# Kernel optimization log

Measured on AMD Instinct MI355X. Metric: run time of the kernel, lower is better.

## Reference

```python
import jax, jax.numpy as jnp
import numpy as np
from jax import lax

PRE_NMS_TOP_N = 2000
POST_NMS_TOP_N = 1000
NMS_THRESH = 0.7
MIN_SIZE = 0.0
BBOX_XFORM_CLIP = float(np.log(1000.0 / 16.0))
NEG = jnp.float32(-1e30)


def setup_inputs() -> dict:
    key = jax.random.key(0)
    k1, k2, k3, k4, k5 = jax.random.split(key, 5)
    N, A, H, W = 16, 3, 256, 336
    img_h, img_w = 1024, 1344
    num = A * H * W  # 258048 anchors per image
    objectness = jax.random.normal(k1, (N, A, H, W), jnp.float32)
    box_regression = jax.random.normal(k2, (N, A * 4, H, W), jnp.float32) * 0.5
    # synthetic but valid xyxy anchors (x2 > x1, y2 > y1)
    cx = jax.random.uniform(k3, (N, num)) * img_w
    cy = jax.random.uniform(k4, (N, num)) * img_h
    wh = 16.0 + jax.random.uniform(k5, (N, num, 2)) * 256.0
    anchors = jnp.stack([cx - 0.5 * wh[..., 0], cy - 0.5 * wh[..., 1],
                         cx + 0.5 * wh[..., 0], cy + 0.5 * wh[..., 1]], axis=-1)
    return {"anchors": anchors.astype(jnp.float32), "objectness": objectness,
            "box_regression": box_regression, "img_h": img_h, "img_w": img_w}


def box_decode(codes, anchors):
    # BoxCoder(weights=(1,1,1,1)).decode, TO_REMOVE=1 convention
    w = anchors[..., 2] - anchors[..., 0] + 1.0
    h = anchors[..., 3] - anchors[..., 1] + 1.0
    ctr_x = anchors[..., 0] + 0.5 * w
    ctr_y = anchors[..., 1] + 0.5 * h
    dx, dy, dw, dh = codes[..., 0], codes[..., 1], codes[..., 2], codes[..., 3]
    dw = jnp.minimum(dw, BBOX_XFORM_CLIP)
    dh = jnp.minimum(dh, BBOX_XFORM_CLIP)
    pcx = dx * w + ctr_x
    pcy = dy * h + ctr_y
    pw = jnp.exp(dw) * w
    ph = jnp.exp(dh) * h
    return jnp.stack([pcx - 0.5 * pw, pcy - 0.5 * ph,
                      pcx + 0.5 * pw - 1.0, pcy + 0.5 * ph - 1.0], axis=-1)


def pairwise_iou(boxes):
    area = (boxes[:, 2] - boxes[:, 0] + 1.0) * (boxes[:, 3] - boxes[:, 1] + 1.0)
    lt = jnp.maximum(boxes[:, None, :2], boxes[None, :, :2])  # [K,K,2]
    rb = jnp.minimum(boxes[:, None, 2:], boxes[None, :, 2:])
    wh = jnp.maximum(rb - lt + 1.0, 0.0)
    inter = wh[..., 0] * wh[..., 1]
    return inter / (area[:, None] + area[None, :] - inter)


def nms_keep(boxes, valid):
    # boxes already sorted by score desc; greedy suppression scan over rows
    K = boxes.shape[0]
    iou = pairwise_iou(boxes)  # [K,K]
    idx = jnp.arange(K)

    def body(keep, xs):
        row, i = xs
        sup = keep[i] & (idx > i) & (row > NMS_THRESH)
        return keep & ~sup, None

    keep, _ = lax.scan(body, valid, (iou, idx))
    return keep


def reference(anchors, objectness, box_regression, img_h, img_w):
    N, A, H, W = objectness.shape
    # permute_and_flatten: (N,A,H,W) -> (N, H*W*A)
    obj = jax.nn.sigmoid(jnp.transpose(objectness, (0, 2, 3, 1)).reshape(N, -1))
    breg = jnp.transpose(box_regression.reshape(N, A, 4, H, W), (0, 3, 4, 1, 2)).reshape(N, -1, 4)
    k = min(PRE_NMS_TOP_N, obj.shape[1])
    scores, topk_idx = lax.top_k(obj, k)  # sorted desc
    batch = jnp.arange(N)[:, None]
    breg = breg[batch, topk_idx]        # [N,k,4]
    anc = anchors[batch, topk_idx]      # [N,k,4]
    boxes = box_decode(breg, anc)       # [N,k,4]
    # clip_to_image (TO_REMOVE=1)
    x1 = jnp.clip(boxes[..., 0], 0.0, img_w - 1)
    y1 = jnp.clip(boxes[..., 1], 0.0, img_h - 1)
    x2 = jnp.clip(boxes[..., 2], 0.0, img_w - 1)
    y2 = jnp.clip(boxes[..., 3], 0.0, img_h - 1)
    boxes = jnp.stack([x1, y1, x2, y2], axis=-1)
    # remove_small_boxes as a validity mask (fixed shape)
    ws = x2 - x1 + 1.0
    hs = y2 - y1 + 1.0
    valid = (ws >= MIN_SIZE) & (hs >= MIN_SIZE)
    keep = jax.vmap(nms_keep)(boxes, valid)  # [N,k]
    masked = jnp.where(keep, scores, NEG)
    final_scores, sel = lax.top_k(masked, POST_NMS_TOP_N)  # preserves score order
    final_boxes = boxes[batch, sel]
    # [N, post_nms_top_n, 5]: xyxy + objectness (padded slots have score ~ -1e30)
    return jnp.concatenate([final_boxes, final_scores[..., None]], axis=-1)
```

## Files before the change

kernel.cpp:

```cpp
#include <hip/hip_runtime.h>
#include <stdint.h>

#define NIMG 16
#define AANCH 3
#define HH 256
#define WW 336
#define HWP (HH*WW)
#define NUM (AANCH*HWP)
#define TOTAL (NIMG*NUM)
#define PRE_K 2000
#define POST_K 1000
#define NMS_TH 0.7f
#define NEGV -1e30f
#define CAND_CAP 4096
#define ROWS 2048
#define RWORDS 64
#define CHUNK 4096
#define CBLOCKS (NUM / CHUNK)
#define HPARTS 16
#define HBINS 4096
#define HCHUNK (NUM / HPARTS)

#define WS_HIST 0u
#define WS_COLT 0u
#define WS_CBOX 262144u
#define WS_CSCO 1310720u
#define WS_CUT  4194304u
#define WS_CNT  4194560u
#define WS_CAND 4194816u
#define WS_BOX  4719104u
#define WS_SCO  5243392u
#define WS_RMI  5374464u
#define WS_SEL  5378560u
#define WS_MASK 5444096u

__device__ __forceinline__ uint32_t fkey(float f){
    uint32_t b = __float_as_uint(f);
    return (b & 0x80000000u) ? ~b : (b | 0x80000000u);
}
__device__ __forceinline__ float keyf(uint32_t k){
    uint32_t b = (k & 0x80000000u) ? (k & 0x7FFFFFFFu) : ~k;
    return __uint_as_float(b);
}

__global__ __launch_bounds__(1024) void k_hist(const float* __restrict__ obj,
                                               uint32_t* __restrict__ part,
                                               uint32_t* __restrict__ cnt,
                                               uint32_t* __restrict__ rminit){
    int img = blockIdx.x >> 4;
    int blk = blockIdx.x & 15;
    int tid = threadIdx.x;
    if (blockIdx.x == 0){
        for (int i = tid; i < 32 + NIMG * RWORDS; i += 1024){
            if (i < 32) cnt[i] = 0u;
            else        rminit[i - 32] = 0u;
        }
    }
    __shared__ uint32_t h[HBINS];
    #pragma unroll
    for (int i = 0; i < HBINS / 1024; ++i) h[tid + i * 1024] = 0u;
    __syncthreads();
    const float* base = obj + (size_t)img * NUM + (size_t)blk * HCHUNK;
    for (int e = tid * 4; e < HCHUNK; e += 4096){
        float4 v = *(const float4*)(base + e);
        atomicAdd(&h[fkey(v.x) >> 20], 1u);
        atomicAdd(&h[fkey(v.y) >> 20], 1u);
        atomicAdd(&h[fkey(v.z) >> 20], 1u);
        atomicAdd(&h[fkey(v.w) >> 20], 1u);
    }
    __syncthreads();
    uint32_t* p = part + ((size_t)blockIdx.x) * HBINS;
    #pragma unroll
    for (int i = 0; i < HBINS / 1024; ++i) p[tid + i * 1024] = h[tid + i * 1024];
}

__global__ __launch_bounds__(1024) void k_binsel(const uint32_t* __restrict__ part,
                                                 uint32_t* __restrict__ cut,
                                                 uint32_t* __restrict__ nAout){
    int img = blockIdx.x, tid = threadIdx.x;
    const uint32_t* pb = part + (size_t)img * HPARTS * HBINS;
    int bin0 = HBINS - 4 * (tid + 1);
    uint32_t c0 = 0, c1 = 0, c2 = 0, c3 = 0;
    for (int k = 0; k < HPARTS; ++k){
        const uint4 v = *(const uint4*)(pb + (size_t)k * HBINS + bin0);
        c0 += v.x; c1 += v.y; c2 += v.z; c3 += v.w;
    }
    uint32_t s = c0 + c1 + c2 + c3;
    __shared__ uint32_t ss[1024];
    uint32_t x = s;
    ss[tid] = x; __syncthreads();
    for (int d = 1; d < 1024; d <<= 1){
        uint32_t y = (tid >= d) ? ss[tid - d] : 0u;
        __syncthreads();
        x += y; ss[tid] = x;
        __syncthreads();
    }
    uint32_t incl = x, excl = x - s;
    if (excl < PRE_K && incl >= PRE_K){
        uint32_t c = excl;
        uint32_t cc[4] = {c0, c1, c2, c3};
        for (int j = 3; j >= 0; --j){
            uint32_t cb = c;
            c += cc[j];
            if (c >= PRE_K){
                cut[img] = ((uint32_t)(bin0 + j)) << 20;
                nAout[img] = cb;
                break;
            }
        }
    }
}

__device__ __forceinline__ void emit_candidate(
        uint32_t key, uint32_t f, uint32_t pos, int img,
        const float* __restrict__ anchors, const float* __restrict__ breg,
        float imw, float imh,
        unsigned long long* __restrict__ cand,
        float4* __restrict__ cboxes, float* __restrict__ cscores){
    const float CLIPV = 4.135166556742356f;
    cand[img * CAND_CAP + pos] = ((unsigned long long)key << 32)
        | ((unsigned long long)((~f) & 0x3FFFFu) << 14) | (unsigned long long)pos;
    float logit = keyf(key);
    float sc = 1.0f / (1.0f + expf(-logit));
    const float* an = anchors + ((size_t)img * NUM + f) * 4;
    float ax1 = an[0], ay1 = an[1], ax2 = an[2], ay2 = an[3];
    int a = (int)(f % AANCH); int hw = (int)(f / AANCH);
    size_t bbase = ((size_t)img * 12 + a * 4) * HWP + (size_t)hw;
    float dx = breg[bbase], dy = breg[bbase + HWP];
    float dw = breg[bbase + 2 * (size_t)HWP], dh = breg[bbase + 3 * (size_t)HWP];
    float aw = ax2 - ax1 + 1.0f, ah = ay2 - ay1 + 1.0f;
    float cx = ax1 + 0.5f * aw, cy = ay1 + 0.5f * ah;
    dw = fminf(dw, CLIPV); dh = fminf(dh, CLIPV);
    float pcx = dx * aw + cx, pcy = dy * ah + cy;
    float pw = expf(dw) * aw, ph = expf(dh) * ah;
    float x1 = pcx - 0.5f * pw, y1 = pcy - 0.5f * ph;
    float x2 = pcx + 0.5f * pw - 1.0f, y2 = pcy + 0.5f * ph - 1.0f;
    x1 = fminf(fmaxf(x1, 0.0f), imw - 1.0f);
    y1 = fminf(fmaxf(y1, 0.0f), imh - 1.0f);
    x2 = fminf(fmaxf(x2, 0.0f), imw - 1.0f);
    y2 = fminf(fmaxf(y2, 0.0f), imh - 1.0f);
    bool valid = ((x2 - x1 + 1.0f) >= 0.0f) && ((y2 - y1 + 1.0f) >= 0.0f);
    cboxes[img * CAND_CAP + pos] = make_float4(x1, y1, x2, y2);
    cscores[img * CAND_CAP + pos] = valid ? sc : -sc;
}

__global__ __launch_bounds__(256) void k_compact(const float* __restrict__ obj,
                                                 const uint32_t* __restrict__ cut,
                                                 const uint32_t* __restrict__ nAarr,
                                                 uint32_t* __restrict__ cnt,
                                                 unsigned long long* __restrict__ cand,
                                                 const float* __restrict__ anchors,
                                                 const float* __restrict__ breg,
                                                 const int* __restrict__ pimh,
                                                 const int* __restrict__ pimw,
                                                 float4* __restrict__ cboxes,
                                                 float* __restrict__ cscores){
    int img   = blockIdx.x / CBLOCKS;
    int chunk = blockIdx.x - img * CBLOCKS;
    int base  = img * NUM + chunk * CHUNK;
    __shared__ uint32_t lcA, lcB, gbA, gbB;
    __shared__ uint2 lbuf[CHUNK];
    if (threadIdx.x == 0){ lcA = 0u; lcB = 0u; }
    __syncthreads();
    uint32_t cutv = cut[img];
    uint32_t cutbin = cutv >> 20;
    float4 v[4];
    #pragma unroll
    for (int it = 0; it < 4; ++it)
        v[it] = *(const float4*)(obj + base + it * 1024 + (int)threadIdx.x * 4);
    #pragma unroll
    for (int it = 0; it < 4; ++it){
        int e = it * 1024 + (int)threadIdx.x * 4;
        float vv[4] = {v[it].x, v[it].y, v[it].z, v[it].w};
        #pragma unroll
        for (int q = 0; q < 4; ++q){
            uint32_t k = fkey(vv[q]);
            if (k >= cutv){
                int r = chunk * CHUNK + e + q;
                int a = r / HWP, hw = r - a * HWP;
                uint32_t f = (uint32_t)(hw * AANCH + a);
                if ((k >> 20) > cutbin){
                    uint32_t p = atomicAdd(&lcA, 1u);
                    lbuf[p] = make_uint2(k, f);
                } else {
                    uint32_t p = atomicAdd(&lcB, 1u);
                    lbuf[CHUNK - 1 - p] = make_uint2(k, f);
                }
            }
        }
    }
    __syncthreads();
    if (threadIdx.x == 0){
        gbA = (lcA > 0u) ? atomicAdd(&cnt[img], lcA) : 0u;
        gbB = (lcB > 0u) ? atomicAdd(&cnt[16 + img], lcB) : 0u;
    }
    __syncthreads();
    uint32_t nA  = nAarr[img];
    uint32_t nAp = (nA + 1u) & ~1u;
    float imw = (float)(*pimw), imh = (float)(*pimh);
    uint32_t na = lcA, ga = gbA, nb = lcB, gb = gbB;
    for (uint32_t t = threadIdx.x; t < na; t += 256u){
        uint32_t pos = ga + t;
        uint2 kf = lbuf[t];
        emit_candidate(kf.x, kf.y, pos, img, anchors, breg, imw, imh,
                       cand, cboxes, cscores);
    }
    for (uint32_t t = threadIdx.x; t < nb; t += 256u){
        uint32_t pos = nAp + gb + t;
        if (pos < CAND_CAP){
            uint2 kf = lbuf[CHUNK - 1 - t];
            emit_candidate(kf.x, kf.y, pos, img, anchors, breg, imw, imh,
                           cand, cboxes, cscores);
        }
    }
}

__global__ __launch_bounds__(256) void k_rank(
        const unsigned long long* __restrict__ cand, const uint32_t* __restrict__ cnt,
        const uint32_t* __restrict__ nAarr,
        const float4* __restrict__ cboxes, const float* __restrict__ cscores,
        float4* __restrict__ boxes_s, float* __restrict__ scores_s,
        uint32_t* __restrict__ rminit){
    int img = blockIdx.x >> 4;
    int b   = blockIdx.x & 15;
    int tid = threadIdx.x;
    int e   = b * 256 + tid;
    uint32_t nA   = nAarr[img];
    uint32_t nAp  = (nA + 1u) & ~1u;
    uint32_t nB   = min(cnt[16 + img], (uint32_t)CAND_CAP - nAp);
    uint32_t end  = nAp + nB;
    uint32_t endp = (end + 1u) & ~1u;
    const unsigned long long* cp = cand + img * CAND_CAP;
    __shared__ alignas(16) unsigned long long tile[CAND_CAP];
    for (int i = tid; i < (int)endp; i += 256){
        bool v = (i < (int)nA) || (i >= (int)nAp && i < (int)end);
        tile[i] = v ? cp[i] : 0ull;
    }
    __syncthreads();
    bool inA = e < (int)nA;
    bool inB = (e >= (int)nAp) && (e < (int)end);
    bool validE = inA || inB;
    unsigned long long mine = validE ? tile[e] : ~0ull;
    int s0 = inA ? 0 : (inB ? (int)(nAp >> 1) : 0);
    int s1 = inA ? (int)(nAp >> 1) : (inB ? (int)(endp >> 1) : 0);
    int rank = inB ? (int)nA : 0;
    const ulonglong2* tile2 = (const ulonglong2*)tile;
    #pragma unroll 8
    for (int i = s0; i < s1; ++i){
        ulonglong2 p = tile2[i];
        rank += (p.x > mine) ? 1 : 0;
        rank += (p.y > mine) ? 1 : 0;
    }
    if (validE && rank < PRE_K){
        float4 bx = cboxes[img * CAND_CAP + e];
        float s   = cscores[img * CAND_CAP + e];
        boxes_s[img * ROWS + rank] = bx;
        scores_s[img * ROWS + rank] = fabsf(s);
        if (s < 0.0f) atomicOr(&rminit[img * RWORDS + (rank >> 5)], 1u << (rank & 31));
    }
}

__global__ __launch_bounds__(64) void k_diag(const float4* __restrict__ boxes_s,
                                             unsigned long long* __restrict__ colT){
    int img = blockIdx.x >> 5;
    int b   = blockIdx.x & 31;
    int j   = threadIdx.x;
    __shared__ float4 B[64];
    __shared__ float  AR[64];
    float4 bj = boxes_s[img * ROWS + b * 64 + j];
    float aj = (bj.z - bj.x + 1.0f) * (bj.w - bj.y + 1.0f);
    B[j] = bj; AR[j] = aj;
    __syncthreads();
    unsigned long long col = 0ull;
    #pragma unroll 8
    for (int i = 0; i < 64; ++i){
        float4 bi = B[i]; float ai = AR[i];
        float xx1 = fmaxf(bi.x, bj.x), yy1 = fmaxf(bi.y, bj.y);
        float xx2 = fminf(bi.z, bj.z), yy2 = fminf(bi.w, bj.w);
        float iw = fmaxf(xx2 - xx1 + 1.0f, 0.0f);
        float ih = fmaxf(yy2 - yy1 + 1.0f, 0.0f);
        float inter = iw * ih;
        bool pred = (i < j) && (inter > NMS_TH * (ai + aj - inter));
        col |= pred ? (1ull << i) : 0ull;
    }
    colT[(size_t)(img * 32 + b) * 64 + j] = col;
}

__global__ __launch_bounds__(1024) void k_mask(const float4* __restrict__ boxes_s,
                                               uint32_t* __restrict__ mask){
    int img = blockIdx.x >> 4;
    int rc  = blockIdx.x & 15;
    int tid = threadIdx.x;
    int lane = tid & 63;
    int wv = tid >> 6;
    int gw = rc * 16 + wv;
    __shared__ float4 B[PRE_K];
    __shared__ float  AR[PRE_K];
    const float4* bp = boxes_s + img * ROWS;
    for (int t = tid; t < PRE_K; t += 1024){
        float4 b = bp[t]; B[t] = b;
        AR[t] = (b.z - b.x + 1.0f) * (b.w - b.y + 1.0f);
    }
    __syncthreads();
    uint32_t* M = mask + (size_t)img * ROWS * RWORDS;
    for (int i = gw; i < PRE_K; i += 256){
        float4 bi = B[i];
        float ai = AR[i];
        unsigned long long* Mrow = (unsigned long long*)(M + (size_t)i * RWORDS);
        for (int jb = (i >> 6); jb < 32; ++jb){
            int j = (jb << 6) + lane;
            bool pred = false;
            if (j > i && j < PRE_K){
                float4 bj = B[j];
                float xx1 = fmaxf(bi.x, bj.x), yy1 = fmaxf(bi.y, bj.y);
                float xx2 = fminf(bi.z, bj.z), yy2 = fminf(bi.w, bj.w);
                float iw = fmaxf(xx2 - xx1 + 1.0f, 0.0f);
                float ih = fmaxf(yy2 - yy1 + 1.0f, 0.0f);
                float inter = iw * ih;
                pred = inter > NMS_TH * (ai + AR[j] - inter);
            }
            unsigned long long bm = __ballot(pred);
            if (lane == 0) Mrow[jb] = bm;
        }
    }
}

__global__ __launch_bounds__(64) void k_scan(const uint32_t* __restrict__ mask,
                                             const unsigned long long* __restrict__ colT,
                                             const uint32_t* __restrict__ rminit,
                                             const float4* __restrict__ boxes_s,
                                             const float* __restrict__ scores_s,
                                             float* __restrict__ out){
    int img = blockIdx.x; int lane = threadIdx.x;
    const uint32_t* M = mask + (size_t)img * ROWS * RWORDS;
    const unsigned long long* CT = colT + (size_t)img * 32 * 64;
    __shared__ uint32_t S[POST_K];
    uint32_t rm = rminit[img * RWORDS + lane];
    if (lane == 62) rm |= 0xFFFF0000u;
    if (lane == 63) rm  = 0xFFFFFFFFu;
    unsigned long long col = CT[lane];
    #pragma unroll 1
    for (int b = 0; b < 32; ++b){
        const uint32_t* Mb = M + (size_t)(b * 64) * RWORDS + lane;
        uint32_t mrow[64];
        #pragma unroll
        for (int i = 0; i < 64; ++i) mrow[i] = Mb[(size_t)i * RWORDS];
        unsigned long long coln = (b < 31) ? CT[(size_t)(b + 1) * 64 + lane] : 0ull;
        uint32_t lo = __shfl(rm, 2 * b), hi = __shfl(rm, 2 * b + 1);
        unsigned long long inc = ((unsigned long long)hi << 32) | (unsigned long long)lo;
        bool alivej = ((inc >> lane) & 1ull) == 0ull;
        unsigned long long keep = ~inc;
        #pragma unroll 1
        for (int it = 0; it < 66; ++it){
            bool ok = alivej && ((col & keep) == 0ull);
            unsigned long long nk = __ballot(ok);
            if (nk == keep) break;
            keep = nk;
        }
        uint32_t acc = 0u;
        #pragma unroll
        for (int i = 0; i < 64; ++i)
            acc |= (keep & (1ull << i)) ? mrow[i] : 0u;
        rm |= (lane >= 2 * b) ? acc : 0u;
        unsigned long long rmb = ~keep;
        if (lane == 2 * b)     rm = (uint32_t)rmb;
        if (lane == 2 * b + 1) rm = (uint32_t)(rmb >> 32);
        col = coln;
    }
    uint32_t inr = (lane < 62) ? 0xFFFFFFFFu : (lane == 62 ? 0x0000FFFFu : 0u);
    uint32_t kw = (~rm) & inr;
    uint32_t sw = rm & inr;
    uint32_t kc = __popc(kw);
    uint32_t x = kc;
    for (int d = 1; d < 64; d <<= 1){ uint32_t y = __shfl_up(x, d); if (lane >= d) x += y; }
    uint32_t kexcl = x - kc;
    uint32_t ktot = __shfl(x, 63);
    uint32_t m = kw; uint32_t r = 0;
    while (m){
        int b = __ffs(m) - 1;
        uint32_t slot = kexcl + r;
        if (slot < POST_K) S[slot] = (uint32_t)(lane * 32 + b) | 0x80000000u;
        m &= m - 1; ++r;
    }
    if (ktot < POST_K){
        uint32_t sc2 = __popc(sw);
        uint32_t x2 = sc2;
        for (int d = 1; d < 64; d <<= 1){ uint32_t y = __shfl_up(x2, d); if (lane >= d) x2 += y; }
        uint32_t sexcl = x2 - sc2;
        uint32_t m2 = sw; uint32_t r2 = 0;
        while (m2){
            int b = __ffs(m2) - 1;
            uint32_t slot = ktot + sexcl + r2;
            if (slot >= ktot && slot < POST_K) S[slot] = (uint32_t)(lane * 32 + b);
            m2 &= m2 - 1; ++r2;
        }
    }
    __syncthreads();
    const float4* bp = boxes_s + img * ROWS;
    const float* sp = scores_s + img * ROWS;
    float* o = out + (size_t)img * POST_K * 5;
    for (int s = lane; s < POST_K; s += 64){
        uint32_t v = S[s];
        uint32_t pos = v & 0x7FFFFFFFu;
        bool kept = (v >> 31) != 0;
        float4 bx = bp[pos];
        float sc = kept ? sp[pos] : NEGV;
        float* oo = o + s * 5;
        oo[0] = bx.x; oo[1] = bx.y; oo[2] = bx.z; oo[3] = bx.w; oo[4] = sc;
    }
}

extern "C" void kernel_launch(void* const* d_in, const int* in_sizes, int n_in,
                              void* d_out, int out_size, void* d_ws, size_t ws_size,
                              hipStream_t stream) {
    const float* anchors = (const float*)d_in[0];
    const float* obj     = (const float*)d_in[1];
    const float* breg    = (const float*)d_in[2];
    const int*   pimh    = (const int*)d_in[3];
    const int*   pimw    = (const int*)d_in[4];
    float* out = (float*)d_out;
    uint8_t* ws = (uint8_t*)d_ws;

    uint32_t*           part     = (uint32_t*)(ws + WS_HIST);
    unsigned long long* colT     = (unsigned long long*)(ws + WS_COLT);
    float4*             cboxes   = (float4*)(ws + WS_CBOX);
    float*              cscores  = (float*)(ws + WS_CSCO);
    uint32_t*           cut      = (uint32_t*)(ws + WS_CUT);
    uint32_t*           nAarr    = (uint32_t*)(ws + WS_CUT + 64);
    uint32_t*           cnt      = (uint32_t*)(ws + WS_CNT);
    unsigned long long* cand     = (unsigned long long*)(ws + WS_CAND);
    float4*             boxes_s  = (float4*)(ws + WS_BOX);
    float*              scores_s = (float*)(ws + WS_SCO);
    uint32_t*           rminit   = (uint32_t*)(ws + WS_RMI);
    uint32_t*           mask     = (uint32_t*)(ws + WS_MASK);

    k_hist<<<NIMG * HPARTS, 1024, 0, stream>>>(obj, part, cnt, rminit);
    k_binsel<<<NIMG, 1024, 0, stream>>>(part, cut, nAarr);
    k_compact<<<NIMG * CBLOCKS, 256, 0, stream>>>(obj, cut, nAarr, cnt, cand,
                                                  anchors, breg, pimh, pimw,
                                                  cboxes, cscores);
    k_rank<<<NIMG * 16, 256, 0, stream>>>(cand, cnt, nAarr, cboxes, cscores,
                                          boxes_s, scores_s, rminit);
    k_diag<<<NIMG * 32, 64, 0, stream>>>(boxes_s, colT);
    k_mask<<<NIMG * 16, 1024, 0, stream>>>(boxes_s, mask);
    k_scan<<<NIMG, 64, 0, stream>>>(mask, colT, rminit, boxes_s, scores_s, out);
}
```

Before: 148.7 us.

## Double-buffer mask row loads in NMS scan to overlap with the keep fixpoint

The serial per-image scan kernel now keeps two register buffers of 64 mask rows and issues the loads for the next 64-row block before processing the current one, so global-memory latency overlaps the ballot fixpoint iteration. The loop is unrolled by two and launch bounds are set to one block per SM, giving the compiler room for roughly 128 extra VGPRs. This targets the latency-bound sequential chain of 16 single-wave blocks, at the cost of higher register pressure and possible spills.

```diff
diff --git a/kernel.cpp b/kernel.cpp
--- a/kernel.cpp
+++ b/kernel.cpp
@@ -325,12 +325,12 @@
     }
 }
 
-__global__ __launch_bounds__(64) void k_scan(const uint32_t* __restrict__ mask,
-                                             const unsigned long long* __restrict__ colT,
-                                             const uint32_t* __restrict__ rminit,
-                                             const float4* __restrict__ boxes_s,
-                                             const float* __restrict__ scores_s,
-                                             float* __restrict__ out){
+__global__ __launch_bounds__(64, 1) void k_scan(const uint32_t* __restrict__ mask,
+                                                const unsigned long long* __restrict__ colT,
+                                                const uint32_t* __restrict__ rminit,
+                                                const float4* __restrict__ boxes_s,
+                                                const float* __restrict__ scores_s,
+                                                float* __restrict__ out){
     int img = blockIdx.x; int lane = threadIdx.x;
     const uint32_t* M = mask + (size_t)img * ROWS * RWORDS;
     const unsigned long long* CT = colT + (size_t)img * 32 * 64;
@@ -338,35 +338,58 @@
     uint32_t rm = rminit[img * RWORDS + lane];
     if (lane == 62) rm |= 0xFFFF0000u;
     if (lane == 63) rm  = 0xFFFFFFFFu;
-    unsigned long long col = CT[lane];
+
+    uint32_t rowsA[64], rowsB[64];
+    unsigned long long colA, colB;
+    {
+        const uint32_t* Mb = M + lane;
+        colA = CT[lane];
+        #pragma unroll
+        for (int i = 0; i < 64; ++i) rowsA[i] = Mb[(size_t)i * RWORDS];
+    }
+
+#define PHASE(B, ROWSX, COLX)                                                   \
+    {                                                                           \
+        uint32_t lo = __shfl(rm, 2 * (B)), hi = __shfl(rm, 2 * (B) + 1);        \
+        unsigned long long inc = ((unsigned long long)hi << 32)                 \
+                               | (unsigned long long)lo;                        \
+        bool alivej = ((inc >> lane) & 1ull) == 0ull;                           \
+        unsigned long long keep = ~inc;                                         \
+        for (int it = 0; it < 66; ++it){                                        \
+            bool ok = alivej && ((COLX & keep) == 0ull);                        \
+            unsigned long long nk = __ballot(ok);                               \
+            if (nk == keep) break;                                              \
+            keep = nk;                                                          \
+        }                                                                       \
+        uint32_t acc = 0u;                                                      \
+        _Pragma("unroll")                                                       \
+        for (int i = 0; i < 64; ++i)                                            \
+            acc |= (keep & (1ull << i)) ? ROWSX[i] : 0u;                        \
+        rm |= (lane >= 2 * (B)) ? acc : 0u;                                     \
+        unsigned long long rmb = ~keep;                                         \
+        if (lane == 2 * (B))     rm = (uint32_t)rmb;                            \
+        if (lane == 2 * (B) + 1) rm = (uint32_t)(rmb >> 32);                    \
+    }
+
     #pragma unroll 1
-    for (int b = 0; b < 32; ++b){
-        const uint32_t* Mb = M + (size_t)(b * 64) * RWORDS + lane;
-        uint32_t mrow[64];
-        #pragma unroll
-        for (int i = 0; i < 64; ++i) mrow[i] = Mb[(size_t)i * RWORDS];
-        unsigned long long coln = (b < 31) ? CT[(size_t)(b + 1) * 64 + lane] : 0ull;
-        uint32_t lo = __shfl(rm, 2 * b), hi = __shfl(rm, 2 * b + 1);
-        unsigned long long inc = ((unsigned long long)hi << 32) | (unsigned long long)lo;
-        bool alivej = ((inc >> lane) & 1ull) == 0ull;
-        unsigned long long keep = ~inc;
-        #pragma unroll 1
-        for (int it = 0; it < 66; ++it){
-            bool ok = alivej && ((col & keep) == 0ull);
-            unsigned long long nk = __ballot(ok);
-            if (nk == keep) break;
-            keep = nk;
-        }
-        uint32_t acc = 0u;
-        #pragma unroll
-        for (int i = 0; i < 64; ++i)
-            acc |= (keep & (1ull << i)) ? mrow[i] : 0u;
-        rm |= (lane >= 2 * b) ? acc : 0u;
-        unsigned long long rmb = ~keep;
-        if (lane == 2 * b)     rm = (uint32_t)rmb;
-        if (lane == 2 * b + 1) rm = (uint32_t)(rmb >> 32);
-        col = coln;
-    }
+    for (int b = 0; b < 32; b += 2){
+        {
+            const uint32_t* Mb = M + (size_t)((b + 1) * 64) * RWORDS + lane;
+            colB = CT[(size_t)(b + 1) * 64 + lane];
+            #pragma unroll
+            for (int i = 0; i < 64; ++i) rowsB[i] = Mb[(size_t)i * RWORDS];
+        }
+        PHASE(b, rowsA, colA);
+        if (b + 2 < 32){
+            const uint32_t* Mb = M + (size_t)((b + 2) * 64) * RWORDS + lane;
+            colA = CT[(size_t)(b + 2) * 64 + lane];
+            #pragma unroll
+            for (int i = 0; i < 64; ++i) rowsA[i] = Mb[(size_t)i * RWORDS];
+        }
+        PHASE(b + 1, rowsB, colB);
+    }
+#undef PHASE
+
     uint32_t inr = (lane < 62) ? 0xFFFFFFFFu : (lane == 62 ? 0x0000FFFFu : 0u);
     uint32_t kw = (~rm) & inr;
     uint32_t sw = rm & inr;
```

After: 149.0 us. No clear change (+0.2%).
